# Kernel optimization log

Measured on AMD Instinct MI355X. Metric: run time of the kernel, lower is better.

The kernel has to match this reference:

```python
import jax, jax.numpy as jnp
import numpy as np

B, T, D = 4, 4096, 1024
N, L = 2048, 768
H = 16
EPS = 1e-5

def layernorm(x, g, b):
    mu = jnp.mean(x, axis=-1, keepdims=True)
    var = jnp.mean((x - mu) ** 2, axis=-1, keepdims=True)
    return (x - mu) * jax.lax.rsqrt(var + EPS) * g + b

def setup_inputs() -> dict:
    key = jax.random.key(0)
    ks = jax.random.split(key, 8)
    s_d = 1.0 / np.sqrt(D)
    s_l = 1.0 / np.sqrt(L)
    return {
        "x1": jax.random.normal(ks[0], (B, T, D), jnp.float32),
        "x2": jax.random.normal(ks[1], (B, N, L), jnp.float32),
        "Wq": jax.random.normal(ks[2], (D, D), jnp.float32) * s_d,
        "bq": jnp.zeros((D,), jnp.float32),
        "Wk": jax.random.normal(ks[3], (L, D), jnp.float32) * s_l,
        "bk": jnp.zeros((D,), jnp.float32),
        "Wv": jax.random.normal(ks[4], (L, D), jnp.float32) * s_l,
        "bv": jnp.zeros((D,), jnp.float32),
        "Wh": jax.random.normal(ks[5], (D, D), jnp.float32) * s_d,
        "bh": jnp.zeros((D,), jnp.float32),
        "g1": jnp.ones((D,), jnp.float32),
        "b1": jnp.zeros((D,), jnp.float32),
        "g2": jnp.ones((L,), jnp.float32),
        "b2": jnp.zeros((L,), jnp.float32),
    }

def reference(x1, x2, Wq, bq, Wk, bk, Wv, bv, Wh, bh, g1, b1, g2, b2):
    nx1 = layernorm(x1, g1, b1)
    nx2 = layernorm(x2, g2, b2)
    q = (nx1 @ Wq + bq).reshape(B, T, H, D // H)
    k = (nx2 @ Wk + bk).reshape(B, N, H, D // H)
    v = (nx2 @ Wv + bv).reshape(B, N, H, D // H)
    q = jax.nn.softmax(q, axis=-1)
    k = jax.nn.softmax(k, axis=-1)
    # dropout p=0 -> identity
    attn = jnp.einsum('bnhd,bnhl->bhdl', k, v)          # [B,H,dh,dh]
    y = jnp.einsum('bthd,bhdl->bthl', q, attn).reshape(B, T, D)
    return x1 @ Wh + bh + y
```

## Files before the change

### kernel.cpp

```cpp
#include <hip/hip_runtime.h>


#define DEV __device__ __forceinline__

typedef unsigned short bf16_t;
typedef __attribute__((ext_vector_type(8))) __bf16 bf16x8;
typedef __attribute__((ext_vector_type(8))) unsigned short ushort8;
typedef __attribute__((ext_vector_type(4))) float f32x4;

DEV unsigned short f2bf(float f) {
  unsigned int u = __float_as_uint(f);
  unsigned int r = 0x7FFFu + ((u >> 16) & 1u);
  return (unsigned short)((u + r) >> 16);
}
DEV float bf2f(unsigned short u) { return __uint_as_float(((unsigned int)u) << 16); }

DEV void gld16(const void* g, void* l) {
  __builtin_amdgcn_global_load_lds((__attribute__((address_space(1))) void*)g,
                                   (__attribute__((address_space(3))) void*)l, 16, 0, 0);
}

__global__ __launch_bounds__(256) void wprep_kernel(
    const float* __restrict__ Wq, const float* __restrict__ Wk,
    const float* __restrict__ Wv, const float* __restrict__ Wh,
    bf16_t* __restrict__ Wqf, bf16_t* __restrict__ Wkf,
    bf16_t* __restrict__ Wvf, bf16_t* __restrict__ Whf) {
  int t = blockIdx.x;
  const float* src; bf16_t* dst; int KB;
  if (t < 1024)      { src = Wq; dst = Wqf; KB = 32; }
  else if (t < 1792) { src = Wk; dst = Wkf; KB = 24; t -= 1024; }
  else if (t < 2560) { src = Wv; dst = Wvf; KB = 24; t -= 1792; }
  else               { src = Wh; dst = Whf; KB = 32; t -= 2560; }
  int tk = t >> 5, tn = t & 31;
  __shared__ float tile[32][33];
  int tx = threadIdx.x & 31, ty = threadIdx.x >> 5;
#pragma unroll
  for (int i = 0; i < 4; ++i) {
    int r = ty + i * 8;
    tile[r][tx] = src[(size_t)(tk * 32 + r) * 1024 + tn * 32 + tx];
  }
  __syncthreads();
  int tid = threadIdx.x;
  if (tid < 128) {
    int rt = tid >> 6, p = (tid >> 4) & 3, ri = tid & 15;
    ushort8 v;
#pragma unroll
    for (int ko = 0; ko < 8; ++ko)
      v[ko] = f2bf(tile[p * 8 + ko][rt * 16 + ri]);
    size_t off = ((size_t)(tn * 2 + rt) * KB + tk) * 512 + p * 128 + ri * 8;
    *(ushort8*)&dst[off] = v;
  }
}

__global__ __launch_bounds__(256) void ln1_kernel(
    const float* __restrict__ x1, const float* __restrict__ g1, const float* __restrict__ b1,
    bf16_t* __restrict__ nx1f, bf16_t* __restrict__ x1f) {
  __shared__ bf16_t stash[16 * 1032];
  __shared__ float murs[16][2];
  int rt = blockIdx.x, tid = threadIdx.x;
  {
    int rowl = tid >> 4, ci = tid & 15;
    size_t base = ((size_t)rt * 16 + rowl) * 1024;
    float s = 0.f, s2 = 0.f;
#pragma unroll
    for (int j = 0; j < 16; ++j) {
      int k0 = ci * 4 + j * 64;
      float4 f = *(const float4*)&x1[base + k0];
      s += f.x + f.y + f.z + f.w;
      s2 += f.x * f.x + f.y * f.y + f.z * f.z + f.w * f.w;
      ushort4 u;
      u.x = f2bf(f.x); u.y = f2bf(f.y); u.z = f2bf(f.z); u.w = f2bf(f.w);
      *(ushort4*)&stash[rowl * 1032 + k0] = u;
    }
#pragma unroll
    for (int off = 1; off < 16; off <<= 1) {
      s  += __shfl_xor(s, off);
      s2 += __shfl_xor(s2, off);
    }
    if (ci == 0) {
      float mu = s * (1.0f / 1024.0f);
      float var = s2 * (1.0f / 1024.0f) - mu * mu;
      murs[rowl][0] = mu;
      murs[rowl][1] = rsqrtf(var + 1e-5f);
    }
  }
  __syncthreads();
  {
    int ri = tid & 15, pg = tid >> 4;
    float mu = murs[ri][0], rs = murs[ri][1];
#pragma unroll
    for (int t = 0; t < 8; ++t) {
      int P = pg * 8 + t;
      ushort8 raw = *(const ushort8*)&stash[ri * 1032 + P * 8];
      float4 ga = *(const float4*)&g1[P * 8], gb = *(const float4*)&g1[P * 8 + 4];
      float4 ba = *(const float4*)&b1[P * 8], bb = *(const float4*)&b1[P * 8 + 4];
      float gv[8] = {ga.x, ga.y, ga.z, ga.w, gb.x, gb.y, gb.z, gb.w};
      float bv[8] = {ba.x, ba.y, ba.z, ba.w, bb.x, bb.y, bb.z, bb.w};
      ushort8 nv;
#pragma unroll
      for (int ko = 0; ko < 8; ++ko)
        nv[ko] = f2bf((bf2f(raw[ko]) - mu) * rs * gv[ko] + bv[ko]);
      size_t off = ((size_t)rt * 32 + (P >> 2)) * 512 + (P & 3) * 128 + ri * 8;
      *(ushort8*)&nx1f[off] = nv;
      *(ushort8*)&x1f[off] = raw;
    }
  }
}

__global__ __launch_bounds__(256) void ln2_kernel(
    const float* __restrict__ x2, const float* __restrict__ g2, const float* __restrict__ b2,
    bf16_t* __restrict__ nx2f) {
  __shared__ bf16_t stash[16 * 776];
  __shared__ float murs[16][2];
  int rt = blockIdx.x, tid = threadIdx.x;
  {
    int rowl = tid >> 4, ci = tid & 15;
    size_t base = ((size_t)rt * 16 + rowl) * 768;
    float s = 0.f, s2 = 0.f;
#pragma unroll
    for (int j = 0; j < 12; ++j) {
      int k0 = ci * 4 + j * 64;
      float4 f = *(const float4*)&x2[base + k0];
      s += f.x + f.y + f.z + f.w;
      s2 += f.x * f.x + f.y * f.y + f.z * f.z + f.w * f.w;
      ushort4 u;
      u.x = f2bf(f.x); u.y = f2bf(f.y); u.z = f2bf(f.z); u.w = f2bf(f.w);
      *(ushort4*)&stash[rowl * 776 + k0] = u;
    }
#pragma unroll
    for (int off = 1; off < 16; off <<= 1) {
      s  += __shfl_xor(s, off);
      s2 += __shfl_xor(s2, off);
    }
    if (ci == 0) {
      float mu = s * (1.0f / 768.0f);
      float var = s2 * (1.0f / 768.0f) - mu * mu;
      murs[rowl][0] = mu;
      murs[rowl][1] = rsqrtf(var + 1e-5f);
    }
  }
  __syncthreads();
  {
    int ri = tid & 15, pg = tid >> 4;
    float mu = murs[ri][0], rs = murs[ri][1];
#pragma unroll
    for (int t = 0; t < 6; ++t) {
      int P = pg * 6 + t;
      ushort8 raw = *(const ushort8*)&stash[ri * 776 + P * 8];
      float4 ga = *(const float4*)&g2[P * 8], gb = *(const float4*)&g2[P * 8 + 4];
      float4 ba = *(const float4*)&b2[P * 8], bb = *(const float4*)&b2[P * 8 + 4];
      float gv[8] = {ga.x, ga.y, ga.z, ga.w, gb.x, gb.y, gb.z, gb.w};
      float bv[8] = {ba.x, ba.y, ba.z, ba.w, bb.x, bb.y, bb.z, bb.w};
      ushort8 nv;
#pragma unroll
      for (int ko = 0; ko < 8; ++ko)
        nv[ko] = f2bf((bf2f(raw[ko]) - mu) * rs * gv[ko] + bv[ko]);
      size_t off = ((size_t)rt * 24 + (P >> 2)) * 512 + (P & 3) * 128 + ri * 8;
      *(ushort8*)&nx2f[off] = nv;
    }
  }
}

__global__ __launch_bounds__(256, 2) void gemm_qkv_kernel(
    const bf16_t* __restrict__ nx1f, const bf16_t* __restrict__ Wqf,
    const float* __restrict__ bq, bf16_t* __restrict__ qout,
    const bf16_t* __restrict__ nx2f, const bf16_t* __restrict__ Wkf,
    const float* __restrict__ bk, bf16_t* __restrict__ kout,
    const bf16_t* __restrict__ Wvf, const float* __restrict__ bv,
    bf16_t* __restrict__ vout) {
  __shared__ bf16_t Bs[2 * 16 * 512];
  int id = blockIdx.x;
  const bf16_t *A, *BT; const float* bias; bf16_t* out;
  int nk, bm, bn, do_softmax;
  if (id < 512) {
    A = nx1f; BT = Wqf; bias = bq; out = qout; nk = 32;
    bm = id & 127; bn = id >> 7; do_softmax = 1;
  } else if (id < 768) {
    id -= 512; A = nx2f; BT = Wkf; bias = bk; out = kout; nk = 24;
    bm = id & 63; bn = id >> 6; do_softmax = 1;
  } else {
    id -= 768; A = nx2f; BT = Wvf; bias = bv; out = vout; nk = 24;
    bm = id & 63; bn = id >> 6; do_softmax = 0;
  }
  int tid = threadIdx.x, lane = tid & 63, wid = tid >> 6;
  int wm = wid & 1, wn = wid >> 1;

  const bf16_t* ap[4];
#pragma unroll
  for (int mi = 0; mi < 4; ++mi)
    ap[mi] = A + ((size_t)(bm * 8 + wm * 4 + mi) * nk) * 512 + lane * 8;
  const bf16_t* sp[4];
#pragma unroll
  for (int i = 0; i < 4; ++i)
    sp[i] = BT + ((size_t)(bn * 16 + wid * 4 + i) * nk) * 512 + lane * 8;

  f32x4 acc[4][8];
#pragma unroll
  for (int i = 0; i < 4; ++i)
#pragma unroll
    for (int j = 0; j < 8; ++j) acc[i][j] = {0.f, 0.f, 0.f, 0.f};

  bf16x8 acur[4], anxt[4];
#pragma unroll
  for (int i = 0; i < 4; ++i)
    gld16(sp[i], (void*)&Bs[(wid * 4 + i) * 512 + lane * 8]);
#pragma unroll
  for (int mi = 0; mi < 4; ++mi) acur[mi] = *(const bf16x8*)ap[mi];

  for (int kt = 0; kt < nk; ++kt) {
    int cb = kt & 1;
    if (kt + 1 < nk) {
      int nb = cb ^ 1;
#pragma unroll
      for (int i = 0; i < 4; ++i)
        gld16(sp[i] + (kt + 1) * 512, (void*)&Bs[nb * 8192 + (wid * 4 + i) * 512 + lane * 8]);
#pragma unroll
      for (int mi = 0; mi < 4; ++mi) anxt[mi] = *(const bf16x8*)(ap[mi] + (kt + 1) * 512);
      asm volatile("s_waitcnt vmcnt(8)\n\ts_barrier" ::: "memory");
    } else {
      asm volatile("s_waitcnt vmcnt(0)\n\ts_barrier" ::: "memory");
    }
    bf16x8 bfr[8];
#pragma unroll
    for (int ni = 0; ni < 8; ++ni)
      bfr[ni] = *(const bf16x8*)&Bs[cb * 8192 + (wn * 8 + ni) * 512 + lane * 8];
#pragma unroll
    for (int mi = 0; mi < 4; ++mi)
#pragma unroll
      for (int ni = 0; ni < 8; ++ni)
        acc[mi][ni] = __builtin_amdgcn_mfma_f32_16x16x32_bf16(acur[mi], bfr[ni], acc[mi][ni], 0, 0, 0);
    asm volatile("s_waitcnt lgkmcnt(0)\n\ts_barrier" ::: "memory");
#pragma unroll
    for (int mi = 0; mi < 4; ++mi) acur[mi] = anxt[mi];
  }

  int colg0 = bn * 256 + wn * 128;
  float bvv[8];
#pragma unroll
  for (int ni = 0; ni < 8; ++ni) bvv[ni] = bias[colg0 + ni * 16 + (lane & 15)];
#pragma unroll
  for (int mi = 0; mi < 4; ++mi) {
#pragma unroll
    for (int r = 0; r < 4; ++r) {
      int row = bm * 128 + wm * 64 + mi * 16 + (lane >> 4) * 4 + r;
      float vx[8];
#pragma unroll
      for (int ni = 0; ni < 8; ++ni) vx[ni] = acc[mi][ni][r] + bvv[ni];
      if (do_softmax) {
#pragma unroll
        for (int g = 0; g < 2; ++g) {
          float ssum = 0.f;
#pragma unroll
          for (int j = 0; j < 4; ++j) { vx[g * 4 + j] = __expf(vx[g * 4 + j]); ssum += vx[g * 4 + j]; }
#pragma unroll
          for (int off = 1; off < 16; off <<= 1) ssum += __shfl_xor(ssum, off);
          float inv = 1.0f / ssum;
#pragma unroll
          for (int j = 0; j < 4; ++j) vx[g * 4 + j] *= inv;
        }
      }
#pragma unroll
      for (int ni = 0; ni < 8; ++ni)
        out[(size_t)row * 1024 + colg0 + ni * 16 + (lane & 15)] = f2bf(vx[ni]);
    }
  }
}

__global__ __launch_bounds__(256) void attn_partial_kernel(
    const bf16_t* __restrict__ kq, const bf16_t* __restrict__ vq,
    float* __restrict__ part) {
  int bh = blockIdx.x >> 3, c = blockIdx.x & 7;
  int b = bh >> 4, h = bh & 15;
  int tid = threadIdx.x;
  int td = tid & 15, tl = tid >> 4;
  __shared__ float ks[32][64];
  __shared__ float vs[32][64];
  float acc[4][4];
#pragma unroll
  for (int i = 0; i < 4; ++i)
#pragma unroll
    for (int j = 0; j < 4; ++j) acc[i][j] = 0.f;
  for (int s = 0; s < 8; ++s) {
    __syncthreads();
    int nr = tid >> 3, col = (tid & 7) * 8;
    int n = c * 256 + s * 32 + nr;
    size_t goff = ((size_t)(b * 2048 + n)) * 1024 + h * 64 + col;
    ushort8 lk = *(const ushort8*)&kq[goff];
    ushort8 lv = *(const ushort8*)&vq[goff];
#pragma unroll
    for (int j = 0; j < 8; ++j) {
      ks[nr][col + j] = bf2f(lk[j]);
      vs[nr][col + j] = bf2f(lv[j]);
    }
    __syncthreads();
#pragma unroll
    for (int nn = 0; nn < 32; ++nn) {
      float4 kv = *(const float4*)&ks[nn][td * 4];
      float4 vv = *(const float4*)&vs[nn][tl * 4];
      float ka[4] = {kv.x, kv.y, kv.z, kv.w};
      float va[4] = {vv.x, vv.y, vv.z, vv.w};
#pragma unroll
      for (int i = 0; i < 4; ++i)
#pragma unroll
        for (int j = 0; j < 4; ++j) acc[i][j] += ka[i] * va[j];
    }
  }
#pragma unroll
  for (int i = 0; i < 4; ++i)
#pragma unroll
    for (int j = 0; j < 4; ++j) {
      int d = td * 4 + i, l = tl * 4 + j;
      part[(((size_t)bh * 8 + c) * 64 + d) * 64 + l] = acc[i][j];
    }
}

__global__ __launch_bounds__(256) void attn_finalize_kernel(
    const float* __restrict__ part, bf16_t* __restrict__ attnT) {
  int bh = blockIdx.x, tid = threadIdx.x;
  for (int t = tid; t < 4096; t += 256) {
    int d = t >> 6, l = t & 63;
    float s = 0.f;
#pragma unroll
    for (int c = 0; c < 8; ++c)
      s += part[(((size_t)bh * 8 + c) * 64 + d) * 64 + l];
    attnT[((size_t)bh * 64 + l) * 64 + d] = f2bf(s);
  }
}

__global__ __launch_bounds__(256, 2) void gemm_final_kernel(
    const bf16_t* __restrict__ x1f, const bf16_t* __restrict__ Whf,
    const float* __restrict__ bias, const bf16_t* __restrict__ qb,
    const bf16_t* __restrict__ attnT, float* __restrict__ out) {
  __shared__ bf16_t Bs[2 * 16 * 512];
  const int nk = 32;
  int tid = threadIdx.x;
  int bm = blockIdx.x, bn = blockIdx.y;
  int lane = tid & 63, wid = tid >> 6;
  int wm = wid & 1, wn = wid >> 1;
  int b = bm >> 5;
  int klane = (lane >> 4) * 8;

  const bf16_t* ap[4];
#pragma unroll
  for (int mi = 0; mi < 4; ++mi)
    ap[mi] = x1f + ((size_t)(bm * 8 + wm * 4 + mi) * nk) * 512 + lane * 8;
  const bf16_t* sp[4];
#pragma unroll
  for (int i = 0; i < 4; ++i)
    sp[i] = Whf + ((size_t)(bn * 16 + wid * 4 + i) * nk) * 512 + lane * 8;

  f32x4 acc[4][8];
#pragma unroll
  for (int i = 0; i < 4; ++i)
#pragma unroll
    for (int j = 0; j < 8; ++j) acc[i][j] = {0.f, 0.f, 0.f, 0.f};

  bf16x8 acur[4], anxt[4];
#pragma unroll
  for (int i = 0; i < 4; ++i)
    gld16(sp[i], (void*)&Bs[(wid * 4 + i) * 512 + lane * 8]);
#pragma unroll
  for (int mi = 0; mi < 4; ++mi) acur[mi] = *(const bf16x8*)ap[mi];

  for (int kt = 0; kt < nk; ++kt) {
    int cb = kt & 1;
    if (kt + 1 < nk) {
      int nb = cb ^ 1;
#pragma unroll
      for (int i = 0; i < 4; ++i)
        gld16(sp[i] + (kt + 1) * 512, (void*)&Bs[nb * 8192 + (wid * 4 + i) * 512 + lane * 8]);
#pragma unroll
      for (int mi = 0; mi < 4; ++mi) anxt[mi] = *(const bf16x8*)(ap[mi] + (kt + 1) * 512);
      asm volatile("s_waitcnt vmcnt(8)\n\ts_barrier" ::: "memory");
    } else {
      asm volatile("s_waitcnt vmcnt(0)\n\ts_barrier" ::: "memory");
    }
    bf16x8 bfr[8];
#pragma unroll
    for (int ni = 0; ni < 8; ++ni)
      bfr[ni] = *(const bf16x8*)&Bs[cb * 8192 + (wn * 8 + ni) * 512 + lane * 8];
#pragma unroll
    for (int mi = 0; mi < 4; ++mi)
#pragma unroll
      for (int ni = 0; ni < 8; ++ni)
        acc[mi][ni] = __builtin_amdgcn_mfma_f32_16x16x32_bf16(acur[mi], bfr[ni], acc[mi][ni], 0, 0, 0);
    asm volatile("s_waitcnt lgkmcnt(0)\n\ts_barrier" ::: "memory");
#pragma unroll
    for (int mi = 0; mi < 4; ++mi) acur[mi] = anxt[mi];
  }

  {
    int h0 = bn * 4 + wn * 2;
#pragma unroll
    for (int k2 = 0; k2 < 2; ++k2) {
      bf16x8 aq[2][4], bt[8];
#pragma unroll
      for (int g = 0; g < 2; ++g)
#pragma unroll
        for (int mi = 0; mi < 4; ++mi)
          aq[g][mi] = *(const bf16x8*)(qb
              + (size_t)(bm * 128 + wm * 64 + mi * 16 + (lane & 15)) * 1024
              + (h0 + g) * 64 + k2 * 32 + klane);
#pragma unroll
      for (int ni = 0; ni < 8; ++ni)
        bt[ni] = *(const bf16x8*)(attnT
            + ((size_t)(b * 16 + h0 + (ni >> 2)) * 64 + (ni & 3) * 16 + (lane & 15)) * 64
            + k2 * 32 + klane);
#pragma unroll
      for (int mi = 0; mi < 4; ++mi)
#pragma unroll
        for (int ni = 0; ni < 8; ++ni)
          acc[mi][ni] = __builtin_amdgcn_mfma_f32_16x16x32_bf16(aq[ni >> 2][mi], bt[ni], acc[mi][ni], 0, 0, 0);
    }
  }

  int colg0 = bn * 256 + wn * 128;
  float bvv[8];
#pragma unroll
  for (int ni = 0; ni < 8; ++ni) bvv[ni] = bias[colg0 + ni * 16 + (lane & 15)];
#pragma unroll
  for (int mi = 0; mi < 4; ++mi)
#pragma unroll
    for (int r = 0; r < 4; ++r) {
      int row = bm * 128 + wm * 64 + mi * 16 + (lane >> 4) * 4 + r;
#pragma unroll
      for (int ni = 0; ni < 8; ++ni)
        out[(size_t)row * 1024 + colg0 + ni * 16 + (lane & 15)] = acc[mi][ni][r] + bvv[ni];
    }
}

extern "C" void kernel_launch(void* const* d_in, const int* in_sizes, int n_in,
                              void* d_out, int out_size, void* d_ws, size_t ws_size,
                              hipStream_t stream) {
  const float* x1 = (const float*)d_in[0];
  const float* x2 = (const float*)d_in[1];
  const float* Wq = (const float*)d_in[2];
  const float* bq = (const float*)d_in[3];
  const float* Wk = (const float*)d_in[4];
  const float* bk = (const float*)d_in[5];
  const float* Wv = (const float*)d_in[6];
  const float* bv = (const float*)d_in[7];
  const float* Wh = (const float*)d_in[8];
  const float* bh = (const float*)d_in[9];
  const float* g1 = (const float*)d_in[10];
  const float* b1 = (const float*)d_in[11];
  const float* g2 = (const float*)d_in[12];
  const float* b2 = (const float*)d_in[13];
  float* out = (float*)d_out;

  char* w = (char*)d_ws;
  bf16_t* nx1f = (bf16_t*)w; w += (size_t)16384 * 1024 * 2;
  bf16_t* x1f  = (bf16_t*)w; w += (size_t)16384 * 1024 * 2;
  bf16_t* nx2f = (bf16_t*)w; w += (size_t)8192 * 768 * 2;
  bf16_t* Wqf  = (bf16_t*)w; w += (size_t)1024 * 1024 * 2;
  bf16_t* Wkf  = (bf16_t*)w; w += (size_t)1024 * 768 * 2;
  bf16_t* Wvf  = (bf16_t*)w; w += (size_t)1024 * 768 * 2;
  bf16_t* Whf  = (bf16_t*)w; w += (size_t)1024 * 1024 * 2;
  bf16_t* qb   = (bf16_t*)w; w += (size_t)16384 * 1024 * 2;
  bf16_t* kbuf = (bf16_t*)w; w += (size_t)8192 * 1024 * 2;
  bf16_t* vbuf = (bf16_t*)w; w += (size_t)8192 * 1024 * 2;
  float*  part = (float*)w;  w += (size_t)64 * 8 * 64 * 64 * 4;
  bf16_t* attnT = (bf16_t*)w; w += (size_t)64 * 64 * 64 * 2;

  wprep_kernel<<<dim3(3584), dim3(256), 0, stream>>>(Wq, Wk, Wv, Wh, Wqf, Wkf, Wvf, Whf);
  ln1_kernel<<<dim3(1024), dim3(256), 0, stream>>>(x1, g1, b1, nx1f, x1f);
  ln2_kernel<<<dim3(512), dim3(256), 0, stream>>>(x2, g2, b2, nx2f);
  gemm_qkv_kernel<<<dim3(1024), dim3(256), 0, stream>>>(
      nx1f, Wqf, bq, qb, nx2f, Wkf, bk, kbuf, Wvf, bv, vbuf);
  attn_partial_kernel<<<dim3(512), dim3(256), 0, stream>>>(kbuf, vbuf, part);
  attn_finalize_kernel<<<dim3(64), dim3(256), 0, stream>>>(part, attnT);
  gemm_final_kernel<<<dim3(128, 4), dim3(256), 0, stream>>>(x1f, Whf, bh, qb, attnT, out);
}
```

Measured before the change: 316.0 us.

## Fuse prep kernels, deepen GEMM B-tile pipeline, replace attn finalize with atomics

Merges weight conversion and both layernorms into one launch, and replaces the partial-sum finalize kernel with fp32 atomicAdd into a memset-zeroed buffer; the final GEMM converts those fp32 values to bf16 when loading. Both GEMMs switch to a 4-slot LDS ring with two-tile-ahead async B loads, and drop the post-compute barrier. The aim is fewer launches and better hiding of load latency. In exchange, LDS use doubles, atomics add contention, and the attention reads in the final GEMM become wider.

```diff
diff --git a/kernel.cpp b/kernel.cpp
--- a/kernel.cpp
+++ b/kernel.cpp
@@ -20,143 +20,148 @@
                                    (__attribute__((address_space(3))) void*)l, 16, 0, 0);
 }
 
-__global__ __launch_bounds__(256) void wprep_kernel(
+DEV bf16x8 cvtf8(float4 a, float4 b) {
+  ushort8 u;
+  u[0] = f2bf(a.x); u[1] = f2bf(a.y); u[2] = f2bf(a.z); u[3] = f2bf(a.w);
+  u[4] = f2bf(b.x); u[5] = f2bf(b.y); u[6] = f2bf(b.z); u[7] = f2bf(b.w);
+  return *(bf16x8*)&u;
+}
+
+__global__ __launch_bounds__(256) void prep_kernel(
     const float* __restrict__ Wq, const float* __restrict__ Wk,
     const float* __restrict__ Wv, const float* __restrict__ Wh,
     bf16_t* __restrict__ Wqf, bf16_t* __restrict__ Wkf,
-    bf16_t* __restrict__ Wvf, bf16_t* __restrict__ Whf) {
-  int t = blockIdx.x;
-  const float* src; bf16_t* dst; int KB;
-  if (t < 1024)      { src = Wq; dst = Wqf; KB = 32; }
-  else if (t < 1792) { src = Wk; dst = Wkf; KB = 24; t -= 1024; }
-  else if (t < 2560) { src = Wv; dst = Wvf; KB = 24; t -= 1792; }
-  else               { src = Wh; dst = Whf; KB = 32; t -= 2560; }
-  int tk = t >> 5, tn = t & 31;
-  __shared__ float tile[32][33];
-  int tx = threadIdx.x & 31, ty = threadIdx.x >> 5;
-#pragma unroll
-  for (int i = 0; i < 4; ++i) {
-    int r = ty + i * 8;
-    tile[r][tx] = src[(size_t)(tk * 32 + r) * 1024 + tn * 32 + tx];
-  }
-  __syncthreads();
-  int tid = threadIdx.x;
-  if (tid < 128) {
-    int rt = tid >> 6, p = (tid >> 4) & 3, ri = tid & 15;
-    ushort8 v;
-#pragma unroll
-    for (int ko = 0; ko < 8; ++ko)
-      v[ko] = f2bf(tile[p * 8 + ko][rt * 16 + ri]);
-    size_t off = ((size_t)(tn * 2 + rt) * KB + tk) * 512 + p * 128 + ri * 8;
-    *(ushort8*)&dst[off] = v;
-  }
-}
-
-__global__ __launch_bounds__(256) void ln1_kernel(
-    const float* __restrict__ x1, const float* __restrict__ g1, const float* __restrict__ b1,
-    bf16_t* __restrict__ nx1f, bf16_t* __restrict__ x1f) {
-  __shared__ bf16_t stash[16 * 1032];
-  __shared__ float murs[16][2];
-  int rt = blockIdx.x, tid = threadIdx.x;
-  {
-    int rowl = tid >> 4, ci = tid & 15;
-    size_t base = ((size_t)rt * 16 + rowl) * 1024;
-    float s = 0.f, s2 = 0.f;
-#pragma unroll
-    for (int j = 0; j < 16; ++j) {
-      int k0 = ci * 4 + j * 64;
-      float4 f = *(const float4*)&x1[base + k0];
-      s += f.x + f.y + f.z + f.w;
-      s2 += f.x * f.x + f.y * f.y + f.z * f.z + f.w * f.w;
-      ushort4 u;
-      u.x = f2bf(f.x); u.y = f2bf(f.y); u.z = f2bf(f.z); u.w = f2bf(f.w);
-      *(ushort4*)&stash[rowl * 1032 + k0] = u;
-    }
-#pragma unroll
-    for (int off = 1; off < 16; off <<= 1) {
-      s  += __shfl_xor(s, off);
-      s2 += __shfl_xor(s2, off);
-    }
-    if (ci == 0) {
-      float mu = s * (1.0f / 1024.0f);
-      float var = s2 * (1.0f / 1024.0f) - mu * mu;
-      murs[rowl][0] = mu;
-      murs[rowl][1] = rsqrtf(var + 1e-5f);
-    }
-  }
-  __syncthreads();
-  {
-    int ri = tid & 15, pg = tid >> 4;
-    float mu = murs[ri][0], rs = murs[ri][1];
-#pragma unroll
-    for (int t = 0; t < 8; ++t) {
-      int P = pg * 8 + t;
-      ushort8 raw = *(const ushort8*)&stash[ri * 1032 + P * 8];
-      float4 ga = *(const float4*)&g1[P * 8], gb = *(const float4*)&g1[P * 8 + 4];
-      float4 ba = *(const float4*)&b1[P * 8], bb = *(const float4*)&b1[P * 8 + 4];
-      float gv[8] = {ga.x, ga.y, ga.z, ga.w, gb.x, gb.y, gb.z, gb.w};
-      float bv[8] = {ba.x, ba.y, ba.z, ba.w, bb.x, bb.y, bb.z, bb.w};
-      ushort8 nv;
+    bf16_t* __restrict__ Wvf, bf16_t* __restrict__ Whf,
+    const float* __restrict__ x1, const float* __restrict__ g1,
+    const float* __restrict__ b1, bf16_t* __restrict__ nx1f, bf16_t* __restrict__ x1f,
+    const float* __restrict__ x2, const float* __restrict__ g2,
+    const float* __restrict__ b2, bf16_t* __restrict__ nx2f) {
+  __shared__ __align__(16) char smem[33152];
+  int id = blockIdx.x, tid = threadIdx.x;
+  if (id < 3584) {
+    const float* src; bf16_t* dst; int KB; int t = id;
+    if (t < 1024)      { src = Wq; dst = Wqf; KB = 32; }
+    else if (t < 1792) { src = Wk; dst = Wkf; KB = 24; t -= 1024; }
+    else if (t < 2560) { src = Wv; dst = Wvf; KB = 24; t -= 1792; }
+    else               { src = Wh; dst = Whf; KB = 32; t -= 2560; }
+    int tk = t >> 5, tn = t & 31;
+    float (*tile)[33] = (float(*)[33])smem;
+    int tx = tid & 31, ty = tid >> 5;
+#pragma unroll
+    for (int i = 0; i < 4; ++i) {
+      int r = ty + i * 8;
+      tile[r][tx] = src[(size_t)(tk * 32 + r) * 1024 + tn * 32 + tx];
+    }
+    __syncthreads();
+    if (tid < 128) {
+      int rt = tid >> 6, p = (tid >> 4) & 3, ri = tid & 15;
+      ushort8 v;
 #pragma unroll
       for (int ko = 0; ko < 8; ++ko)
-        nv[ko] = f2bf((bf2f(raw[ko]) - mu) * rs * gv[ko] + bv[ko]);
-      size_t off = ((size_t)rt * 32 + (P >> 2)) * 512 + (P & 3) * 128 + ri * 8;
-      *(ushort8*)&nx1f[off] = nv;
-      *(ushort8*)&x1f[off] = raw;
-    }
-  }
-}
-
-__global__ __launch_bounds__(256) void ln2_kernel(
-    const float* __restrict__ x2, const float* __restrict__ g2, const float* __restrict__ b2,
-    bf16_t* __restrict__ nx2f) {
-  __shared__ bf16_t stash[16 * 776];
-  __shared__ float murs[16][2];
-  int rt = blockIdx.x, tid = threadIdx.x;
-  {
-    int rowl = tid >> 4, ci = tid & 15;
-    size_t base = ((size_t)rt * 16 + rowl) * 768;
-    float s = 0.f, s2 = 0.f;
-#pragma unroll
-    for (int j = 0; j < 12; ++j) {
-      int k0 = ci * 4 + j * 64;
-      float4 f = *(const float4*)&x2[base + k0];
-      s += f.x + f.y + f.z + f.w;
-      s2 += f.x * f.x + f.y * f.y + f.z * f.z + f.w * f.w;
-      ushort4 u;
-      u.x = f2bf(f.x); u.y = f2bf(f.y); u.z = f2bf(f.z); u.w = f2bf(f.w);
-      *(ushort4*)&stash[rowl * 776 + k0] = u;
-    }
-#pragma unroll
-    for (int off = 1; off < 16; off <<= 1) {
-      s  += __shfl_xor(s, off);
-      s2 += __shfl_xor(s2, off);
-    }
-    if (ci == 0) {
-      float mu = s * (1.0f / 768.0f);
-      float var = s2 * (1.0f / 768.0f) - mu * mu;
-      murs[rowl][0] = mu;
-      murs[rowl][1] = rsqrtf(var + 1e-5f);
-    }
-  }
-  __syncthreads();
-  {
-    int ri = tid & 15, pg = tid >> 4;
-    float mu = murs[ri][0], rs = murs[ri][1];
-#pragma unroll
-    for (int t = 0; t < 6; ++t) {
-      int P = pg * 6 + t;
-      ushort8 raw = *(const ushort8*)&stash[ri * 776 + P * 8];
-      float4 ga = *(const float4*)&g2[P * 8], gb = *(const float4*)&g2[P * 8 + 4];
-      float4 ba = *(const float4*)&b2[P * 8], bb = *(const float4*)&b2[P * 8 + 4];
-      float gv[8] = {ga.x, ga.y, ga.z, ga.w, gb.x, gb.y, gb.z, gb.w};
-      float bv[8] = {ba.x, ba.y, ba.z, ba.w, bb.x, bb.y, bb.z, bb.w};
-      ushort8 nv;
-#pragma unroll
-      for (int ko = 0; ko < 8; ++ko)
-        nv[ko] = f2bf((bf2f(raw[ko]) - mu) * rs * gv[ko] + bv[ko]);
-      size_t off = ((size_t)rt * 24 + (P >> 2)) * 512 + (P & 3) * 128 + ri * 8;
-      *(ushort8*)&nx2f[off] = nv;
+        v[ko] = f2bf(tile[p * 8 + ko][rt * 16 + ri]);
+      size_t off = ((size_t)(tn * 2 + rt) * KB + tk) * 512 + p * 128 + ri * 8;
+      *(ushort8*)&dst[off] = v;
+    }
+  } else if (id < 4608) {
+    int rt = id - 3584;
+    bf16_t* stash = (bf16_t*)smem;
+    float* murs = (float*)(smem + 33024);
+    {
+      int rowl = tid >> 4, ci = tid & 15;
+      size_t base = ((size_t)rt * 16 + rowl) * 1024;
+      float s = 0.f, s2 = 0.f;
+#pragma unroll
+      for (int j = 0; j < 16; ++j) {
+        int k0 = ci * 4 + j * 64;
+        float4 f = *(const float4*)&x1[base + k0];
+        s += f.x + f.y + f.z + f.w;
+        s2 += f.x * f.x + f.y * f.y + f.z * f.z + f.w * f.w;
+        ushort4 u;
+        u.x = f2bf(f.x); u.y = f2bf(f.y); u.z = f2bf(f.z); u.w = f2bf(f.w);
+        *(ushort4*)&stash[rowl * 1032 + k0] = u;
+      }
+#pragma unroll
+      for (int off = 1; off < 16; off <<= 1) {
+        s  += __shfl_xor(s, off);
+        s2 += __shfl_xor(s2, off);
+      }
+      if (ci == 0) {
+        float mu = s * (1.0f / 1024.0f);
+        float var = s2 * (1.0f / 1024.0f) - mu * mu;
+        murs[rowl * 2] = mu;
+        murs[rowl * 2 + 1] = rsqrtf(var + 1e-5f);
+      }
+    }
+    __syncthreads();
+    {
+      int ri = tid & 15, pg = tid >> 4;
+      float mu = murs[ri * 2], rs = murs[ri * 2 + 1];
+#pragma unroll
+      for (int t = 0; t < 8; ++t) {
+        int P = pg * 8 + t;
+        ushort8 raw = *(const ushort8*)&stash[ri * 1032 + P * 8];
+        float4 ga = *(const float4*)&g1[P * 8], gb = *(const float4*)&g1[P * 8 + 4];
+        float4 ba = *(const float4*)&b1[P * 8], bb = *(const float4*)&b1[P * 8 + 4];
+        float gv[8] = {ga.x, ga.y, ga.z, ga.w, gb.x, gb.y, gb.z, gb.w};
+        float bv[8] = {ba.x, ba.y, ba.z, ba.w, bb.x, bb.y, bb.z, bb.w};
+        ushort8 nv;
+#pragma unroll
+        for (int ko = 0; ko < 8; ++ko)
+          nv[ko] = f2bf((bf2f(raw[ko]) - mu) * rs * gv[ko] + bv[ko]);
+        size_t off = ((size_t)rt * 32 + (P >> 2)) * 512 + (P & 3) * 128 + ri * 8;
+        *(ushort8*)&nx1f[off] = nv;
+        *(ushort8*)&x1f[off] = raw;
+      }
+    }
+  } else {
+    int rt = id - 4608;
+    bf16_t* stash = (bf16_t*)smem;
+    float* murs = (float*)(smem + 25000);
+    {
+      int rowl = tid >> 4, ci = tid & 15;
+      size_t base = ((size_t)rt * 16 + rowl) * 768;
+      float s = 0.f, s2 = 0.f;
+#pragma unroll
+      for (int j = 0; j < 12; ++j) {
+        int k0 = ci * 4 + j * 64;
+        float4 f = *(const float4*)&x2[base + k0];
+        s += f.x + f.y + f.z + f.w;
+        s2 += f.x * f.x + f.y * f.y + f.z * f.z + f.w * f.w;
+        ushort4 u;
+        u.x = f2bf(f.x); u.y = f2bf(f.y); u.z = f2bf(f.z); u.w = f2bf(f.w);
+        *(ushort4*)&stash[rowl * 776 + k0] = u;
+      }
+#pragma unroll
+      for (int off = 1; off < 16; off <<= 1) {
+        s  += __shfl_xor(s, off);
+        s2 += __shfl_xor(s2, off);
+      }
+      if (ci == 0) {
+        float mu = s * (1.0f / 768.0f);
+        float var = s2 * (1.0f / 768.0f) - mu * mu;
+        murs[rowl * 2] = mu;
+        murs[rowl * 2 + 1] = rsqrtf(var + 1e-5f);
+      }
+    }
+    __syncthreads();
+    {
+      int ri = tid & 15, pg = tid >> 4;
+      float mu = murs[ri * 2], rs = murs[ri * 2 + 1];
+#pragma unroll
+      for (int t = 0; t < 6; ++t) {
+        int P = pg * 6 + t;
+        ushort8 raw = *(const ushort8*)&stash[ri * 776 + P * 8];
+        float4 ga = *(const float4*)&g2[P * 8], gb = *(const float4*)&g2[P * 8 + 4];
+        float4 ba = *(const float4*)&b2[P * 8], bb = *(const float4*)&b2[P * 8 + 4];
+        float gv[8] = {ga.x, ga.y, ga.z, ga.w, gb.x, gb.y, gb.z, gb.w};
+        float bv[8] = {ba.x, ba.y, ba.z, ba.w, bb.x, bb.y, bb.z, bb.w};
+        ushort8 nv;
+#pragma unroll
+        for (int ko = 0; ko < 8; ++ko)
+          nv[ko] = f2bf((bf2f(raw[ko]) - mu) * rs * gv[ko] + bv[ko]);
+        size_t off = ((size_t)rt * 24 + (P >> 2)) * 512 + (P & 3) * 128 + ri * 8;
+        *(ushort8*)&nx2f[off] = nv;
+      }
     }
   }
 }
@@ -168,7 +173,7 @@
     const float* __restrict__ bk, bf16_t* __restrict__ kout,
     const bf16_t* __restrict__ Wvf, const float* __restrict__ bv,
     bf16_t* __restrict__ vout) {
-  __shared__ bf16_t Bs[2 * 16 * 512];
+  __shared__ bf16_t Bs[4 * 16 * 512];
   int id = blockIdx.x;
   const bf16_t *A, *BT; const float* bias; bf16_t* out;
   int nk, bm, bn, do_softmax;
@@ -205,31 +210,34 @@
   for (int i = 0; i < 4; ++i)
     gld16(sp[i], (void*)&Bs[(wid * 4 + i) * 512 + lane * 8]);
 #pragma unroll
+  for (int i = 0; i < 4; ++i)
+    gld16(sp[i] + 512, (void*)&Bs[8192 + (wid * 4 + i) * 512 + lane * 8]);
+#pragma unroll
   for (int mi = 0; mi < 4; ++mi) acur[mi] = *(const bf16x8*)ap[mi];
 
   for (int kt = 0; kt < nk; ++kt) {
-    int cb = kt & 1;
+    if (kt + 2 < nk) {
+#pragma unroll
+      for (int i = 0; i < 4; ++i)
+        gld16(sp[i] + (size_t)(kt + 2) * 512,
+              (void*)&Bs[((kt + 2) & 3) * 8192 + (wid * 4 + i) * 512 + lane * 8]);
+    }
     if (kt + 1 < nk) {
-      int nb = cb ^ 1;
-#pragma unroll
-      for (int i = 0; i < 4; ++i)
-        gld16(sp[i] + (kt + 1) * 512, (void*)&Bs[nb * 8192 + (wid * 4 + i) * 512 + lane * 8]);
-#pragma unroll
-      for (int mi = 0; mi < 4; ++mi) anxt[mi] = *(const bf16x8*)(ap[mi] + (kt + 1) * 512);
-      asm volatile("s_waitcnt vmcnt(8)\n\ts_barrier" ::: "memory");
-    } else {
-      asm volatile("s_waitcnt vmcnt(0)\n\ts_barrier" ::: "memory");
-    }
+#pragma unroll
+      for (int mi = 0; mi < 4; ++mi) anxt[mi] = *(const bf16x8*)(ap[mi] + (size_t)(kt + 1) * 512);
+    }
+    if (kt + 2 < nk)      asm volatile("s_waitcnt vmcnt(8)\n\ts_barrier" ::: "memory");
+    else if (kt + 1 < nk) asm volatile("s_waitcnt vmcnt(4)\n\ts_barrier" ::: "memory");
+    else                  asm volatile("s_waitcnt vmcnt(0)\n\ts_barrier" ::: "memory");
     bf16x8 bfr[8];
 #pragma unroll
     for (int ni = 0; ni < 8; ++ni)
-      bfr[ni] = *(const bf16x8*)&Bs[cb * 8192 + (wn * 8 + ni) * 512 + lane * 8];
+      bfr[ni] = *(const bf16x8*)&Bs[(kt & 3) * 8192 + (wn * 8 + ni) * 512 + lane * 8];
 #pragma unroll
     for (int mi = 0; mi < 4; ++mi)
 #pragma unroll
       for (int ni = 0; ni < 8; ++ni)
         acc[mi][ni] = __builtin_amdgcn_mfma_f32_16x16x32_bf16(acur[mi], bfr[ni], acc[mi][ni], 0, 0, 0);
-    asm volatile("s_waitcnt lgkmcnt(0)\n\ts_barrier" ::: "memory");
 #pragma unroll
     for (int mi = 0; mi < 4; ++mi) acur[mi] = anxt[mi];
   }
@@ -268,7 +276,7 @@
 
 __global__ __launch_bounds__(256) void attn_partial_kernel(
     const bf16_t* __restrict__ kq, const bf16_t* __restrict__ vq,
-    float* __restrict__ part) {
+    float* __restrict__ attnF) {
   int bh = blockIdx.x >> 3, c = blockIdx.x & 7;
   int b = bh >> 4, h = bh & 15;
   int tid = threadIdx.x;
@@ -310,28 +318,15 @@
 #pragma unroll
     for (int j = 0; j < 4; ++j) {
       int d = td * 4 + i, l = tl * 4 + j;
-      part[(((size_t)bh * 8 + c) * 64 + d) * 64 + l] = acc[i][j];
-    }
-}
-
-__global__ __launch_bounds__(256) void attn_finalize_kernel(
-    const float* __restrict__ part, bf16_t* __restrict__ attnT) {
-  int bh = blockIdx.x, tid = threadIdx.x;
-  for (int t = tid; t < 4096; t += 256) {
-    int d = t >> 6, l = t & 63;
-    float s = 0.f;
-#pragma unroll
-    for (int c = 0; c < 8; ++c)
-      s += part[(((size_t)bh * 8 + c) * 64 + d) * 64 + l];
-    attnT[((size_t)bh * 64 + l) * 64 + d] = f2bf(s);
-  }
+      atomicAdd(&attnF[(size_t)bh * 4096 + l * 64 + d], acc[i][j]);
+    }
 }
 
 __global__ __launch_bounds__(256, 2) void gemm_final_kernel(
     const bf16_t* __restrict__ x1f, const bf16_t* __restrict__ Whf,
     const float* __restrict__ bias, const bf16_t* __restrict__ qb,
-    const bf16_t* __restrict__ attnT, float* __restrict__ out) {
-  __shared__ bf16_t Bs[2 * 16 * 512];
+    const float* __restrict__ attnF, float* __restrict__ out) {
+  __shared__ bf16_t Bs[4 * 16 * 512];
   const int nk = 32;
   int tid = threadIdx.x;
   int bm = blockIdx.x, bn = blockIdx.y;
@@ -360,31 +355,34 @@
   for (int i = 0; i < 4; ++i)
     gld16(sp[i], (void*)&Bs[(wid * 4 + i) * 512 + lane * 8]);
 #pragma unroll
+  for (int i = 0; i < 4; ++i)
+    gld16(sp[i] + 512, (void*)&Bs[8192 + (wid * 4 + i) * 512 + lane * 8]);
+#pragma unroll
   for (int mi = 0; mi < 4; ++mi) acur[mi] = *(const bf16x8*)ap[mi];
 
   for (int kt = 0; kt < nk; ++kt) {
-    int cb = kt & 1;
+    if (kt + 2 < nk) {
+#pragma unroll
+      for (int i = 0; i < 4; ++i)
+        gld16(sp[i] + (size_t)(kt + 2) * 512,
+              (void*)&Bs[((kt + 2) & 3) * 8192 + (wid * 4 + i) * 512 + lane * 8]);
+    }
     if (kt + 1 < nk) {
-      int nb = cb ^ 1;
-#pragma unroll
-      for (int i = 0; i < 4; ++i)
-        gld16(sp[i] + (kt + 1) * 512, (void*)&Bs[nb * 8192 + (wid * 4 + i) * 512 + lane * 8]);
-#pragma unroll
-      for (int mi = 0; mi < 4; ++mi) anxt[mi] = *(const bf16x8*)(ap[mi] + (kt + 1) * 512);
-      asm volatile("s_waitcnt vmcnt(8)\n\ts_barrier" ::: "memory");
-    } else {
-      asm volatile("s_waitcnt vmcnt(0)\n\ts_barrier" ::: "memory");
-    }
+#pragma unroll
+      for (int mi = 0; mi < 4; ++mi) anxt[mi] = *(const bf16x8*)(ap[mi] + (size_t)(kt + 1) * 512);
+    }
+    if (kt + 2 < nk)      asm volatile("s_waitcnt vmcnt(8)\n\ts_barrier" ::: "memory");
+    else if (kt + 1 < nk) asm volatile("s_waitcnt vmcnt(4)\n\ts_barrier" ::: "memory");
+    else                  asm volatile("s_waitcnt vmcnt(0)\n\ts_barrier" ::: "memory");
     bf16x8 bfr[8];
 #pragma unroll
     for (int ni = 0; ni < 8; ++ni)
-      bfr[ni] = *(const bf16x8*)&Bs[cb * 8192 + (wn * 8 + ni) * 512 + lane * 8];
+      bfr[ni] = *(const bf16x8*)&Bs[(kt & 3) * 8192 + (wn * 8 + ni) * 512 + lane * 8];
 #pragma unroll
     for (int mi = 0; mi < 4; ++mi)
 #pragma unroll
       for (int ni = 0; ni < 8; ++ni)
         acc[mi][ni] = __builtin_amdgcn_mfma_f32_16x16x32_bf16(acur[mi], bfr[ni], acc[mi][ni], 0, 0, 0);
-    asm volatile("s_waitcnt lgkmcnt(0)\n\ts_barrier" ::: "memory");
 #pragma unroll
     for (int mi = 0; mi < 4; ++mi) acur[mi] = anxt[mi];
   }
@@ -402,10 +400,12 @@
               + (size_t)(bm * 128 + wm * 64 + mi * 16 + (lane & 15)) * 1024
               + (h0 + g) * 64 + k2 * 32 + klane);
 #pragma unroll
-      for (int ni = 0; ni < 8; ++ni)
-        bt[ni] = *(const bf16x8*)(attnT
+      for (int ni = 0; ni < 8; ++ni) {
+        const float* p = attnF
             + ((size_t)(b * 16 + h0 + (ni >> 2)) * 64 + (ni & 3) * 16 + (lane & 15)) * 64
-            + k2 * 32 + klane);
+            + k2 * 32 + klane;
+        bt[ni] = cvtf8(*(const float4*)p, *(const float4*)(p + 4));
+      }
 #pragma unroll
       for (int mi = 0; mi < 4; ++mi)
 #pragma unroll
@@ -459,15 +459,14 @@
   bf16_t* qb   = (bf16_t*)w; w += (size_t)16384 * 1024 * 2;
   bf16_t* kbuf = (bf16_t*)w; w += (size_t)8192 * 1024 * 2;
   bf16_t* vbuf = (bf16_t*)w; w += (size_t)8192 * 1024 * 2;
-  float*  part = (float*)w;  w += (size_t)64 * 8 * 64 * 64 * 4;
-  bf16_t* attnT = (bf16_t*)w; w += (size_t)64 * 64 * 64 * 2;
-
-  wprep_kernel<<<dim3(3584), dim3(256), 0, stream>>>(Wq, Wk, Wv, Wh, Wqf, Wkf, Wvf, Whf);
-  ln1_kernel<<<dim3(1024), dim3(256), 0, stream>>>(x1, g1, b1, nx1f, x1f);
-  ln2_kernel<<<dim3(512), dim3(256), 0, stream>>>(x2, g2, b2, nx2f);
+  float*  attnF = (float*)w; w += (size_t)64 * 4096 * 4;
+
+  hipMemsetAsync(attnF, 0, (size_t)64 * 4096 * 4, stream);
+  prep_kernel<<<dim3(5120), dim3(256), 0, stream>>>(
+      Wq, Wk, Wv, Wh, Wqf, Wkf, Wvf, Whf,
+      x1, g1, b1, nx1f, x1f, x2, g2, b2, nx2f);
   gemm_qkv_kernel<<<dim3(1024), dim3(256), 0, stream>>>(
       nx1f, Wqf, bq, qb, nx2f, Wkf, bk, kbuf, Wvf, bv, vbuf);
-  attn_partial_kernel<<<dim3(512), dim3(256), 0, stream>>>(kbuf, vbuf, part);
-  attn_finalize_kernel<<<dim3(64), dim3(256), 0, stream>>>(part, attnT);
-  gemm_final_kernel<<<dim3(128, 4), dim3(256), 0, stream>>>(x1f, Whf, bh, qb, attnT, out);
-}
+  attn_partial_kernel<<<dim3(512), dim3(256), 0, stream>>>(kbuf, vbuf, attnF);
+  gemm_final_kernel<<<dim3(128, 4), dim3(256), 0, stream>>>(x1f, Whf, bh, qb, attnF, out);
+}
```

Measured after the change: 337.8 us. 1.07x slower.
